# Performance work log

Measured on AMD Instinct MI355X. Metric: run time of the kernel, lower is better.

Reference implementation:

```python
import jax, jax.numpy as jnp
import numpy as np

NHEAD = 8
LN_EPS = 1e-5


def _l2norm(x, eps=1e-6):
    # matches torch.nn.functional.normalize(p=2, eps=eps)
    n = jnp.linalg.norm(x, axis=-1, keepdims=True)
    return x / jnp.maximum(n, eps)


def setup_inputs() -> dict:
    key = jax.random.key(0)
    ks = jax.random.split(key, 10)
    Q, B, D = 100, 16, 256
    T, Dc = 8192, 768
    s = lambda d: 1.0 / np.sqrt(d)
    return {
        "tgt": jax.random.normal(ks[0], (Q, B, D), jnp.float32),
        "text_classification": jax.random.normal(ks[1], (B, T, Dc), jnp.float32),
        "query_pos": jax.random.normal(ks[2], (Q, B, D), jnp.float32),
        "out_of_vocab_logits": jax.random.normal(ks[3], (B, Q, T), jnp.float32),
        "Wq": jax.random.normal(ks[4], (D, D), jnp.float32) * s(D),
        "bq": jnp.zeros((D,), jnp.float32),
        "Wk": jax.random.normal(ks[5], (D, Dc), jnp.float32) * s(Dc),
        "bk": jnp.zeros((D,), jnp.float32),
        "Wv": jax.random.normal(ks[6], (D, Dc), jnp.float32) * s(Dc),
        "bv": jnp.zeros((D,), jnp.float32),
        "Wo": jax.random.normal(ks[7], (D, D), jnp.float32) * s(D),
        "bo": jnp.zeros((D,), jnp.float32),
        "ln_g": jnp.ones((D,), jnp.float32),
        "ln_b": jnp.zeros((D,), jnp.float32),
        "log_scale": jnp.asarray(np.log(1.0 / 0.07), jnp.float32),
    }


def reference(tgt, text_classification, query_pos, out_of_vocab_logits,
              Wq, bq, Wk, bk, Wv, bv, Wo, bo, ln_g, ln_b, log_scale):
    Qn, B, D = tgt.shape
    T = text_classification.shape[1]
    H = NHEAD
    hd = D // H

    # forward_post: q = tgt + query_pos ; k = v = text_classification
    q_in = tgt + query_pos                                   # [Q, B, D]
    q = jnp.einsum('qbd,ed->qbe', q_in, Wq) + bq             # [Q, B, D]
    k = jnp.einsum('btc,ec->bte', text_classification, Wk) + bk  # [B, T, D]
    v = jnp.einsum('btc,ec->bte', text_classification, Wv) + bv  # [B, T, D]

    # split heads -> [B, H, L, hd]
    q = q.transpose(1, 0, 2).reshape(B, Qn, H, hd).transpose(0, 2, 1, 3)
    k = k.reshape(B, T, H, hd).transpose(0, 2, 1, 3)
    v = v.reshape(B, T, H, hd).transpose(0, 2, 1, 3)

    q = _l2norm(q)
    k = _l2norm(k)
    scale = jnp.minimum(jnp.exp(log_scale), 100.0)
    logits = jnp.einsum('bhqd,bhkd->bhqk', q, k) * scale     # [B, H, Q, T]

    # per-head ensemble with out-of-vocab logits
    alpha = jnp.linspace(0.0, 1.0, H, dtype=logits.dtype).reshape(1, H, 1, 1)
    logits = logits * (1.0 - alpha) + out_of_vocab_logits[:, None] * alpha

    attn = jax.nn.softmax(logits, axis=-1)
    out = jnp.einsum('bhqk,bhkd->bhqd', attn, v)             # [B, H, Q, hd]
    out = out.transpose(0, 2, 1, 3).reshape(B, Qn, D).transpose(1, 0, 2)  # [Q, B, D]
    out = jnp.einsum('qbd,ed->qbe', out, Wo) + bo

    # residual + LayerNorm (post-norm)
    x = tgt + out
    mu = x.mean(axis=-1, keepdims=True)
    var = x.var(axis=-1, keepdims=True)
    x = (x - mu) * jax.lax.rsqrt(var + LN_EPS) * ln_g + ln_b
    return x
```

## Files before the change

### kernel.cpp

```cpp
#include <hip/hip_runtime.h>
#include <hip/hip_bf16.h>

#define QN 100
#define QP 112
#define BB 16
#define DD 256
#define TT 8192
#define DC 768
#define HH 8
#define HD 32
#define NS 8
#define TSL (TT / NS)

typedef short bf16x4 __attribute__((ext_vector_type(4)));
typedef short bf16x8 __attribute__((ext_vector_type(8)));
typedef float f32x4 __attribute__((ext_vector_type(4)));

__device__ __forceinline__ uint pack_bf16_hi2(float f0, float f1) {
  return (__float_as_uint(f0) >> 16) | (__float_as_uint(f1) & 0xffff0000u);
}

__global__ __launch_bounds__(256) void qproj_kernel(
    const float* __restrict__ tgt, const float* __restrict__ qpos,
    const float* __restrict__ Wq, const float* __restrict__ bq,
    ushort* __restrict__ Qhi, ushort* __restrict__ Qlo) {
  int bid = blockIdx.x;
  int q = bid >> 4, b = bid & 15;
  int e = threadIdx.x;
  int h = e >> 5, d = e & 31;
  size_t widx = ((size_t)(b * HH + h) * QP + q) * HD + d;
  if (q >= QN) { Qhi[widx] = 0; Qlo[widx] = 0; return; }
  __shared__ float arow[DD];
  size_t off = ((size_t)q * BB + b) * DD + e;
  arow[e] = tgt[off] + qpos[off];
  __syncthreads();
  const float4* w4 = (const float4*)(Wq + (size_t)e * DD);
  const float4* a4 = (const float4*)arow;
  float acc = bq[e];
#pragma unroll 8
  for (int i = 0; i < DD / 4; ++i) {
    float4 wv = w4[i], av = a4[i];
    acc += wv.x * av.x + wv.y * av.y + wv.z * av.z + wv.w * av.w;
  }
  float ss = acc * acc;
#pragma unroll
  for (int o = 16; o; o >>= 1) ss += __shfl_xor(ss, o, 64);
  float qn = acc * (1.0f / fmaxf(sqrtf(ss), 1e-6f));
  uint u = __float_as_uint(qn);
  float hif = __uint_as_float(u & 0xffff0000u);
  Qhi[widx] = (ushort)(u >> 16);
  Qlo[widx] = (ushort)(__float_as_uint(qn - hif) >> 16);
}

__global__ __launch_bounds__(256) void kv_gemm_kernel(
    const float* __restrict__ text,
    const float* __restrict__ Wk, const float* __restrict__ bk,
    const float* __restrict__ Wv, const float* __restrict__ bv,
    float* __restrict__ Kout, float* __restrict__ Vout) {
  __shared__ short Ahi[4][129][8];
  __shared__ short Alo[4][129][8];
  __shared__ short Bhi[4][129][8];
  __shared__ short Blo[4][129][8];

  int bid = blockIdx.x;
  int w = (bid & 7) * 512 + (bid >> 3);
  int mt = w >> 2, nt = w & 3;
  int m0 = mt * 128, n0 = nt * 128;
  int tid = threadIdx.x;

  const float* Wbase = (n0 < 256) ? Wk : Wv;
  const float* bias_vec = (n0 < 256) ? bk : bv;
  float* dst = (n0 < 256) ? Kout : Vout;
  int ncol0 = n0 & 255;

  int r = tid & 127;
  bool isA = tid < 128;
  const float* src = isA ? (text + (size_t)(m0 + r) * DC)
                         : (Wbase + (size_t)(ncol0 + r) * DC);
  short (*dhi)[129][8] = isA ? Ahi : Bhi;
  short (*dlo)[129][8] = isA ? Alo : Blo;

  int lane = tid & 63, wid = tid >> 6;
  int wm = wid >> 1, wn = wid & 1;
  int kg = lane >> 4, fr = lane & 15;

  f32x4 acc[4][4];
#pragma unroll
  for (int i = 0; i < 4; ++i)
#pragma unroll
    for (int j = 0; j < 4; ++j) acc[i][j] = (f32x4){0.f, 0.f, 0.f, 0.f};

  float4 ra[8];
#pragma unroll
  for (int c = 0; c < 8; ++c) ra[c] = *(const float4*)(src + c * 4);

  for (int ks = 0; ks < DC / 32; ++ks) {
    const float* raf = (const float*)ra;
#pragma unroll
    for (int g = 0; g < 4; ++g) {
      uint hiw[4], low[4];
#pragma unroll
      for (int p = 0; p < 4; ++p) {
        float f0 = raf[8 * g + 2 * p], f1 = raf[8 * g + 2 * p + 1];
        uint b0 = __float_as_uint(f0), b1 = __float_as_uint(f1);
        float h0 = __uint_as_float(b0 & 0xffff0000u);
        float h1 = __uint_as_float(b1 & 0xffff0000u);
        hiw[p] = (b0 >> 16) | (b1 & 0xffff0000u);
        low[p] = (__float_as_uint(f0 - h0) >> 16) |
                 (__float_as_uint(f1 - h1) & 0xffff0000u);
      }
      *(uint4*)&dhi[g][r][0] = make_uint4(hiw[0], hiw[1], hiw[2], hiw[3]);
      *(uint4*)&dlo[g][r][0] = make_uint4(low[0], low[1], low[2], low[3]);
    }
    __syncthreads();

    if (ks < DC / 32 - 1) {
      const float* s2 = src + (ks + 1) * 32;
#pragma unroll
      for (int c = 0; c < 8; ++c) ra[c] = *(const float4*)(s2 + c * 4);
    }

    bf16x8 bh[4], bl[4];
#pragma unroll
    for (int ni = 0; ni < 4; ++ni) {
      int row = wn * 64 + ni * 16 + fr;
      bh[ni] = *(const bf16x8*)&Bhi[kg][row][0];
      bl[ni] = *(const bf16x8*)&Blo[kg][row][0];
    }
#pragma unroll
    for (int mi = 0; mi < 4; ++mi) {
      int row = wm * 64 + mi * 16 + fr;
      bf16x8 ah = *(const bf16x8*)&Ahi[kg][row][0];
      bf16x8 al = *(const bf16x8*)&Alo[kg][row][0];
#pragma unroll
      for (int ni = 0; ni < 4; ++ni) {
        acc[mi][ni] = __builtin_amdgcn_mfma_f32_16x16x32_bf16(
            ah, bh[ni], acc[mi][ni], 0, 0, 0);
        acc[mi][ni] = __builtin_amdgcn_mfma_f32_16x16x32_bf16(
            ah, bl[ni], acc[mi][ni], 0, 0, 0);
        acc[mi][ni] = __builtin_amdgcn_mfma_f32_16x16x32_bf16(
            al, bh[ni], acc[mi][ni], 0, 0, 0);
      }
    }
    __syncthreads();
  }

#pragma unroll
  for (int ni = 0; ni < 4; ++ni) {
    int col = n0 + wn * 64 + ni * 16 + fr;
    int e = col & 255;
    int h = e >> 5, d = e & 31;
    float bias = bias_vec[e];
#pragma unroll
    for (int mi = 0; mi < 4; ++mi) {
      f32x4 c = acc[mi][ni];
      int mbase = m0 + wm * 64 + mi * 16 + kg * 4;
#pragma unroll
      for (int j = 0; j < 4; ++j) {
        int m = mbase + j;
        int b = m >> 13, t = m & 8191;
        dst[(((size_t)(b * HH + h)) * TT + t) * HD + d] = c[j] + bias;
      }
    }
  }
}

__global__ __launch_bounds__(256) void prep_kernel(float* __restrict__ Kbuf,
                                                   float* __restrict__ Vbuf) {
  __shared__ float vl[32][257];
  int c = blockIdx.x;
  int tid = threadIdx.x;
  float* Kc = Kbuf + (size_t)c * 8192;
  float* Vc = Vbuf + (size_t)c * 8192;

  float kr[32];
#pragma unroll
  for (int i = 0; i < 8; ++i)
    *(float4*)&kr[i * 4] = *(const float4*)(Kc + (size_t)tid * 32 + i * 4);
#pragma unroll
  for (int i = 0; i < 8; ++i) {
    float4 v = *(const float4*)(Vc + (size_t)tid * 32 + i * 4);
    vl[i * 4 + 0][tid] = v.x;
    vl[i * 4 + 1][tid] = v.y;
    vl[i * 4 + 2][tid] = v.z;
    vl[i * 4 + 3][tid] = v.w;
  }
  __syncthreads();

  float ss = 0.f;
#pragma unroll
  for (int i = 0; i < 32; ++i) ss += kr[i] * kr[i];
  float rk = 1.0f / fmaxf(sqrtf(ss), 1e-6f);
  ushort* Kh = (ushort*)Kc;
  uint hiw[16], low[16];
#pragma unroll
  for (int p = 0; p < 16; ++p) {
    float f0 = kr[2 * p] * rk, f1 = kr[2 * p + 1] * rk;
    uint b0 = __float_as_uint(f0), b1 = __float_as_uint(f1);
    float h0 = __uint_as_float(b0 & 0xffff0000u);
    float h1 = __uint_as_float(b1 & 0xffff0000u);
    hiw[p] = (b0 >> 16) | (b1 & 0xffff0000u);
    low[p] = (__float_as_uint(f0 - h0) >> 16) |
             (__float_as_uint(f1 - h1) & 0xffff0000u);
  }
#pragma unroll
  for (int i = 0; i < 4; ++i) {
    *(uint4*)(Kh + (size_t)tid * 32 + i * 8) =
        make_uint4(hiw[4 * i], hiw[4 * i + 1], hiw[4 * i + 2], hiw[4 * i + 3]);
    *(uint4*)(Kh + 8192 + (size_t)tid * 32 + i * 8) =
        make_uint4(low[4 * i], low[4 * i + 1], low[4 * i + 2], low[4 * i + 3]);
  }

  int d = tid & 31, c8 = tid >> 5;
  float vv[32];
#pragma unroll
  for (int t = 0; t < 32; ++t) vv[t] = vl[d][c8 * 32 + t];
  ushort* Vh = (ushort*)Vc;
#pragma unroll
  for (int p = 0; p < 16; ++p) {
    float f0 = vv[2 * p], f1 = vv[2 * p + 1];
    uint b0 = __float_as_uint(f0), b1 = __float_as_uint(f1);
    float h0 = __uint_as_float(b0 & 0xffff0000u);
    float h1 = __uint_as_float(b1 & 0xffff0000u);
    hiw[p] = (b0 >> 16) | (b1 & 0xffff0000u);
    low[p] = (__float_as_uint(f0 - h0) >> 16) |
             (__float_as_uint(f1 - h1) & 0xffff0000u);
  }
#pragma unroll
  for (int i = 0; i < 4; ++i) {
    *(uint4*)(Vh + (size_t)d * 256 + c8 * 32 + i * 8) =
        make_uint4(hiw[4 * i], hiw[4 * i + 1], hiw[4 * i + 2], hiw[4 * i + 3]);
    *(uint4*)(Vh + 8192 + (size_t)d * 256 + c8 * 32 + i * 8) =
        make_uint4(low[4 * i], low[4 * i + 1], low[4 * i + 2], low[4 * i + 3]);
  }
}

__global__ __launch_bounds__(256, 2) void attn_kernel(
    const ushort* __restrict__ Qhi, const ushort* __restrict__ Qlo,
    const ushort* __restrict__ Kpl, const ushort* __restrict__ Vpl,
    const float* __restrict__ oov, const float* __restrict__ log_scale,
    float* __restrict__ pacc, float* __restrict__ pl) {
  __shared__ short Pbuf[4][2][QP][36];
  int bid = blockIdx.x;
  int sl = bid & 7, bh = bid >> 3;
  int b = bh >> 3, h = bh & 7;
  int tid = threadIdx.x, lane = tid & 63, w = tid >> 6;
  int fr = lane & 15, kg = lane >> 4;

  float scale = fminf(__expf(log_scale[0]), 100.0f);
  float alpha = (float)h * (1.0f / 7.0f);
  float cs = scale * (1.0f - alpha);

  bf16x8 qhf[7], qlf[7];
#pragma unroll
  for (int qt = 0; qt < 7; ++qt) {
    size_t qa = ((size_t)bh * QP + qt * 16 + fr) * HD + kg * 8;
    qhf[qt] = *(const bf16x8*)(Qhi + qa);
    qlf[qt] = *(const bf16x8*)(Qlo + qa);
  }

  f32x4 oacc[7][2];
#pragma unroll
  for (int qt = 0; qt < 7; ++qt)
#pragma unroll
    for (int dt = 0; dt < 2; ++dt) oacc[qt][dt] = (f32x4){0.f, 0.f, 0.f, 0.f};
  float lsum[7][4];
#pragma unroll
  for (int qt = 0; qt < 7; ++qt)
#pragma unroll
    for (int j = 0; j < 4; ++j) lsum[qt][j] = 0.f;

  short* Ph = &Pbuf[w][0][0][0];
  short* Pl = &Pbuf[w][1][0][0];
  const float* oovb = oov + (size_t)b * QN * TT;

  for (int s = 0; s < 8; ++s) {
    int t0 = sl * TSL + s * 128 + w * 32;
    int c = bh * 32 + (t0 >> 8);
    int ttb = t0 & 255;
    const ushort* Kc = Kpl + (size_t)c * 16384;
    const ushort* Vc = Vpl + (size_t)c * 16384;

    bf16x8 kh[2], kl[2];
#pragma unroll
    for (int tt = 0; tt < 2; ++tt) {
      int off = (ttb + tt * 16 + fr) * HD + kg * 8;
      kh[tt] = *(const bf16x8*)(Kc + off);
      kl[tt] = *(const bf16x8*)(Kc + 8192 + off);
    }

#pragma unroll
    for (int qt = 0; qt < 7; ++qt) {
#pragma unroll
      for (int tt = 0; tt < 2; ++tt) {
        f32x4 sacc = (f32x4){0.f, 0.f, 0.f, 0.f};
        sacc = __builtin_amdgcn_mfma_f32_16x16x32_bf16(qhf[qt], kh[tt], sacc, 0, 0, 0);
        sacc = __builtin_amdgcn_mfma_f32_16x16x32_bf16(qlf[qt], kh[tt], sacc, 0, 0, 0);
        sacc = __builtin_amdgcn_mfma_f32_16x16x32_bf16(qhf[qt], kl[tt], sacc, 0, 0, 0);
        int tcol = t0 + tt * 16 + fr;
#pragma unroll
        for (int j = 0; j < 4; ++j) {
          int q = qt * 16 + kg * 4 + j;
          int qc = q < QN ? q : QN - 1;
          float ov = oovb[(size_t)qc * TT + tcol];
          float S = __expf(sacc[j] * cs + ov * alpha);
          lsum[qt][j] += S;
          uint u = __float_as_uint(S);
          float hif = __uint_as_float(u & 0xffff0000u);
          Ph[q * 36 + tt * 16 + fr] = (short)(u >> 16);
          Pl[q * 36 + tt * 16 + fr] = (short)(__float_as_uint(S - hif) >> 16);
        }
      }
    }

    bf16x8 vh[2], vlo[2];
#pragma unroll
    for (int dt = 0; dt < 2; ++dt) {
      int off = (dt * 16 + fr) * 256 + ttb + kg * 8;
      vh[dt] = *(const bf16x8*)(Vc + off);
      vlo[dt] = *(const bf16x8*)(Vc + 8192 + off);
    }

#pragma unroll
    for (int qt = 0; qt < 7; ++qt) {
      int qrow = qt * 16 + fr;
      bf16x4 ph0 = *(const bf16x4*)&Ph[qrow * 36 + kg * 8];
      bf16x4 ph1 = *(const bf16x4*)&Ph[qrow * 36 + kg * 8 + 4];
      bf16x4 pl0 = *(const bf16x4*)&Pl[qrow * 36 + kg * 8];
      bf16x4 pl1 = *(const bf16x4*)&Pl[qrow * 36 + kg * 8 + 4];
      bf16x8 pా = __builtin_shufflevector(ph0, ph1, 0, 1, 2, 3, 4, 5, 6, 7);
      bf16x8 plv = __builtin_shufflevector(pl0, pl1, 0, 1, 2, 3, 4, 5, 6, 7);
#pragma unroll
      for (int dt = 0; dt < 2; ++dt) {
        oacc[qt][dt] = __builtin_amdgcn_mfma_f32_16x16x32_bf16(pా, vh[dt], oacc[qt][dt], 0, 0, 0);
        oacc[qt][dt] = __builtin_amdgcn_mfma_f32_16x16x32_bf16(plv, vh[dt], oacc[qt][dt], 0, 0, 0);
        oacc[qt][dt] = __builtin_amdgcn_mfma_f32_16x16x32_bf16(pా, vlo[dt], oacc[qt][dt], 0, 0, 0);
      }
    }
  }

#pragma unroll
  for (int qt = 0; qt < 7; ++qt)
#pragma unroll
    for (int j = 0; j < 4; ++j) {
      float v = lsum[qt][j];
      v += __shfl_xor(v, 1, 64);
      v += __shfl_xor(v, 2, 64);
      v += __shfl_xor(v, 4, 64);
      v += __shfl_xor(v, 8, 64);
      lsum[qt][j] = v;
    }

  float* red = (float*)&Pbuf[w][0][0][0];
#pragma unroll
  for (int qt = 0; qt < 7; ++qt)
#pragma unroll
    for (int dt = 0; dt < 2; ++dt)
#pragma unroll
      for (int j = 0; j < 4; ++j)
        red[(qt * 16 + kg * 4 + j) * HD + dt * 16 + fr] = oacc[qt][dt][j];
  if (fr == 0) {
#pragma unroll
    for (int qt = 0; qt < 7; ++qt)
#pragma unroll
      for (int j = 0; j < 4; ++j)
        red[QP * HD + qt * 16 + kg * 4 + j] = lsum[qt][j];
  }
  __syncthreads();

  const int WSTRIDE = 2 * QP * 36 / 2;
  float* r0 = (float*)&Pbuf[0][0][0][0];
  size_t pbase = ((size_t)bh * NS + sl) * QN;
  for (int idx = tid; idx < QN * HD; idx += 256) {
    int q = idx >> 5, d = idx & 31;
    float ssum = 0.f;
#pragma unroll
    for (int wv = 0; wv < 4; ++wv) ssum += r0[wv * WSTRIDE + (q * HD + d)];
    pacc[(pbase + q) * HD + d] = ssum;
  }
  if (tid < QN) {
    float lt = 0.f;
#pragma unroll
    for (int wv = 0; wv < 4; ++wv) lt += r0[wv * WSTRIDE + QP * HD + tid];
    pl[pbase + tid] = lt;
  }
}

__global__ __launch_bounds__(256) void out_kernel(
    const float* __restrict__ part_acc, const float* __restrict__ part_l,
    const float* __restrict__ Wo, const float* __restrict__ bo,
    const float* __restrict__ tgt, const float* __restrict__ ln_g,
    const float* __restrict__ ln_b, float* __restrict__ out) {
  int bid = blockIdx.x;
  int q = bid >> 4, b = bid & 15;
  int e = threadIdx.x;
  int h = e >> 5, d = e & 31;
  __shared__ float row[DD];
  __shared__ float r1[4], r2[4];

  size_t base = ((size_t)(b * HH + h)) * NS * QN + q;
  float a = 0.0f, lt = 0.0f;
#pragma unroll
  for (int s = 0; s < NS; ++s) {
    a += part_acc[(base + (size_t)s * QN) * HD + d];
    lt += part_l[base + (size_t)s * QN];
  }
  row[e] = a / lt;
  __syncthreads();

  const float4* w4 = (const float4*)(Wo + (size_t)e * DD);
  const float4* r4 = (const float4*)row;
  float o = bo[e];
#pragma unroll 8
  for (int i = 0; i < DD / 4; ++i) {
    float4 wv = w4[i], rv = r4[i];
    o += wv.x * rv.x + wv.y * rv.y + wv.z * rv.z + wv.w * rv.w;
  }
  float x = tgt[((size_t)q * BB + b) * DD + e] + o;

  float s1 = x, s2 = x * x;
#pragma unroll
  for (int off = 32; off; off >>= 1) {
    s1 += __shfl_xor(s1, off, 64);
    s2 += __shfl_xor(s2, off, 64);
  }
  int wid = e >> 6, lane = e & 63;
  if (lane == 0) { r1[wid] = s1; r2[wid] = s2; }
  __syncthreads();
  float T1 = r1[0] + r1[1] + r1[2] + r1[3];
  float T2 = r2[0] + r2[1] + r2[2] + r2[3];
  float mu = T1 * (1.0f / DD);
  float var = T2 * (1.0f / DD) - mu * mu;
  out[((size_t)q * BB + b) * DD + e] =
      (x - mu) * rsqrtf(var + 1e-5f) * ln_g[e] + ln_b[e];
}

extern "C" void kernel_launch(void* const* d_in, const int* in_sizes, int n_in,
                              void* d_out, int out_size, void* d_ws, size_t ws_size,
                              hipStream_t stream) {
  (void)in_sizes; (void)n_in; (void)out_size; (void)ws_size;
  const float* tgt  = (const float*)d_in[0];
  const float* text = (const float*)d_in[1];
  const float* qpos = (const float*)d_in[2];
  const float* oov  = (const float*)d_in[3];
  const float* Wq = (const float*)d_in[4];
  const float* bq = (const float*)d_in[5];
  const float* Wk = (const float*)d_in[6];
  const float* bk = (const float*)d_in[7];
  const float* Wv = (const float*)d_in[8];
  const float* bv = (const float*)d_in[9];
  const float* Wo = (const float*)d_in[10];
  const float* bo = (const float*)d_in[11];
  const float* ln_g = (const float*)d_in[12];
  const float* ln_b = (const float*)d_in[13];
  const float* log_scale = (const float*)d_in[14];
  float* out = (float*)d_out;

  char* wsb = (char*)d_ws;
  ushort* Qhi = (ushort*)wsb;
  ushort* Qlo = Qhi + (size_t)BB * HH * QP * HD;
  float* Kbuf = (float*)(wsb + 2u * 917504u);
  float* Vbuf = Kbuf + (size_t)BB * HH * TT * HD;
  float* pacc = Vbuf + (size_t)BB * HH * TT * HD;
  float* pl   = pacc + (size_t)BB * HH * NS * QN * HD;

  hipLaunchKernelGGL(qproj_kernel, dim3(QP * BB), dim3(DD), 0, stream,
                     tgt, qpos, Wq, bq, Qhi, Qlo);
  hipLaunchKernelGGL(kv_gemm_kernel, dim3(4096), dim3(256), 0, stream,
                     text, Wk, bk, Wv, bv, Kbuf, Vbuf);
  hipLaunchKernelGGL(prep_kernel, dim3(4096), dim3(256), 0, stream,
                     Kbuf, Vbuf);
  hipLaunchKernelGGL(attn_kernel, dim3(BB * HH * NS), dim3(256), 0, stream,
                     (const ushort*)Kbuf ? Qhi : Qhi, Qlo,
                     (const ushort*)Kbuf, (const ushort*)Vbuf,
                     oov, log_scale, pacc, pl);
  hipLaunchKernelGGL(out_kernel, dim3(QN * BB), dim3(DD), 0, stream,
                     pacc, pl, Wo, bo, tgt, ln_g, ln_b, out);
}
```

Baseline: 1.552 ms.

## Transpose oov to fp16, drop P low-part MFMAs, split attention finer

Adds a kernel that transposes out_of_vocab_logits into a [B,T,128] fp16 layout so the attention kernel can load it with vector reads instead of strided fp32 gathers. The attention kernel now keeps P in bf16 only, dropping the low-part MFMA and its shared-memory traffic. It also moves to 128-thread blocks with 16 T-slices and writes per-wave partials, removing the in-block reduction. The KV GEMM loop is manually double-buffered in registers. Precision drops for oov (fp16) and for P (bf16 only), and out_kernel now reduces 32 partials instead of 8.

Measured after the change: 1.385 ms. 1.12x faster.

```diff
diff --git a/kernel.cpp b/kernel.cpp
--- a/kernel.cpp
+++ b/kernel.cpp
@@ -9,16 +9,13 @@
 #define DC 768
 #define HH 8
 #define HD 32
-#define NS 8
-#define TSL (TT / NS)
+#define SL16 16
+#define NPART 32
 
 typedef short bf16x4 __attribute__((ext_vector_type(4)));
 typedef short bf16x8 __attribute__((ext_vector_type(8)));
 typedef float f32x4 __attribute__((ext_vector_type(4)));
-
-__device__ __forceinline__ uint pack_bf16_hi2(float f0, float f1) {
-  return (__float_as_uint(f0) >> 16) | (__float_as_uint(f1) & 0xffff0000u);
-}
+typedef _Float16 half4 __attribute__((ext_vector_type(4)));
 
 __global__ __launch_bounds__(256) void qproj_kernel(
     const float* __restrict__ tgt, const float* __restrict__ qpos,
@@ -52,6 +49,48 @@
   Qlo[widx] = (ushort)(__float_as_uint(qn - hif) >> 16);
 }
 
+#define KV_CONVERT(RAF)                                                       \
+  {                                                                           \
+    const float* raf = (const float*)(RAF);                                   \
+    _Pragma("unroll") for (int g = 0; g < 4; ++g) {                           \
+      uint hiw[4], low[4];                                                    \
+      _Pragma("unroll") for (int p2 = 0; p2 < 4; ++p2) {                      \
+        float f0 = raf[8 * g + 2 * p2], f1 = raf[8 * g + 2 * p2 + 1];         \
+        uint b0 = __float_as_uint(f0), b1 = __float_as_uint(f1);              \
+        float h0 = __uint_as_float(b0 & 0xffff0000u);                         \
+        float h1 = __uint_as_float(b1 & 0xffff0000u);                         \
+        hiw[p2] = (b0 >> 16) | (b1 & 0xffff0000u);                            \
+        low[p2] = (__float_as_uint(f0 - h0) >> 16) |                          \
+                  (__float_as_uint(f1 - h1) & 0xffff0000u);                   \
+      }                                                                       \
+      *(uint4*)&dhi[g][r][0] = make_uint4(hiw[0], hiw[1], hiw[2], hiw[3]);    \
+      *(uint4*)&dlo[g][r][0] = make_uint4(low[0], low[1], low[2], low[3]);    \
+    }                                                                         \
+  }
+
+#define KV_MFMA()                                                             \
+  {                                                                           \
+    bf16x8 bhf[4], blf[4];                                                    \
+    _Pragma("unroll") for (int ni = 0; ni < 4; ++ni) {                        \
+      int row = wn * 64 + ni * 16 + fr;                                       \
+      bhf[ni] = *(const bf16x8*)&Bhi[kg][row][0];                             \
+      blf[ni] = *(const bf16x8*)&Blo[kg][row][0];                             \
+    }                                                                         \
+    _Pragma("unroll") for (int mi = 0; mi < 4; ++mi) {                        \
+      int row = wm * 64 + mi * 16 + fr;                                       \
+      bf16x8 ah = *(const bf16x8*)&Ahi[kg][row][0];                           \
+      bf16x8 al = *(const bf16x8*)&Alo[kg][row][0];                           \
+      _Pragma("unroll") for (int ni = 0; ni < 4; ++ni) {                      \
+        acc[mi][ni] = __builtin_amdgcn_mfma_f32_16x16x32_bf16(                \
+            ah, bhf[ni], acc[mi][ni], 0, 0, 0);                               \
+        acc[mi][ni] = __builtin_amdgcn_mfma_f32_16x16x32_bf16(                \
+            ah, blf[ni], acc[mi][ni], 0, 0, 0);                               \
+        acc[mi][ni] = __builtin_amdgcn_mfma_f32_16x16x32_bf16(                \
+            al, bhf[ni], acc[mi][ni], 0, 0, 0);                               \
+      }                                                                       \
+    }                                                                         \
+  }
+
 __global__ __launch_bounds__(256) void kv_gemm_kernel(
     const float* __restrict__ text,
     const float* __restrict__ Wk, const float* __restrict__ bk,
@@ -90,58 +129,28 @@
 #pragma unroll
     for (int j = 0; j < 4; ++j) acc[i][j] = (f32x4){0.f, 0.f, 0.f, 0.f};
 
-  float4 ra[8];
-#pragma unroll
-  for (int c = 0; c < 8; ++c) ra[c] = *(const float4*)(src + c * 4);
-
-  for (int ks = 0; ks < DC / 32; ++ks) {
-    const float* raf = (const float*)ra;
-#pragma unroll
-    for (int g = 0; g < 4; ++g) {
-      uint hiw[4], low[4];
-#pragma unroll
-      for (int p = 0; p < 4; ++p) {
-        float f0 = raf[8 * g + 2 * p], f1 = raf[8 * g + 2 * p + 1];
-        uint b0 = __float_as_uint(f0), b1 = __float_as_uint(f1);
-        float h0 = __uint_as_float(b0 & 0xffff0000u);
-        float h1 = __uint_as_float(b1 & 0xffff0000u);
-        hiw[p] = (b0 >> 16) | (b1 & 0xffff0000u);
-        low[p] = (__float_as_uint(f0 - h0) >> 16) |
-                 (__float_as_uint(f1 - h1) & 0xffff0000u);
-      }
-      *(uint4*)&dhi[g][r][0] = make_uint4(hiw[0], hiw[1], hiw[2], hiw[3]);
-      *(uint4*)&dlo[g][r][0] = make_uint4(low[0], low[1], low[2], low[3]);
-    }
+  float4 raA[8], raB[8];
+#pragma unroll
+  for (int c = 0; c < 8; ++c) raA[c] = *(const float4*)(src + c * 4);
+
+  for (int ks = 0; ks < 24; ks += 2) {
+    {
+      const float* s2 = src + (ks + 1) * 32;
+#pragma unroll
+      for (int c = 0; c < 8; ++c) raB[c] = *(const float4*)(s2 + c * 4);
+    }
+    KV_CONVERT(raA);
     __syncthreads();
-
-    if (ks < DC / 32 - 1) {
-      const float* s2 = src + (ks + 1) * 32;
-#pragma unroll
-      for (int c = 0; c < 8; ++c) ra[c] = *(const float4*)(s2 + c * 4);
-    }
-
-    bf16x8 bh[4], bl[4];
-#pragma unroll
-    for (int ni = 0; ni < 4; ++ni) {
-      int row = wn * 64 + ni * 16 + fr;
-      bh[ni] = *(const bf16x8*)&Bhi[kg][row][0];
-      bl[ni] = *(const bf16x8*)&Blo[kg][row][0];
-    }
-#pragma unroll
-    for (int mi = 0; mi < 4; ++mi) {
-      int row = wm * 64 + mi * 16 + fr;
-      bf16x8 ah = *(const bf16x8*)&Ahi[kg][row][0];
-      bf16x8 al = *(const bf16x8*)&Alo[kg][row][0];
-#pragma unroll
-      for (int ni = 0; ni < 4; ++ni) {
-        acc[mi][ni] = __builtin_amdgcn_mfma_f32_16x16x32_bf16(
-            ah, bh[ni], acc[mi][ni], 0, 0, 0);
-        acc[mi][ni] = __builtin_amdgcn_mfma_f32_16x16x32_bf16(
-            ah, bl[ni], acc[mi][ni], 0, 0, 0);
-        acc[mi][ni] = __builtin_amdgcn_mfma_f32_16x16x32_bf16(
-            al, bh[ni], acc[mi][ni], 0, 0, 0);
-      }
-    }
+    KV_MFMA();
+    __syncthreads();
+    if (ks + 2 < 24) {
+      const float* s3 = src + (ks + 2) * 32;
+#pragma unroll
+      for (int c = 0; c < 8; ++c) raA[c] = *(const float4*)(s3 + c * 4);
+    }
+    KV_CONVERT(raB);
+    __syncthreads();
+    KV_MFMA();
     __syncthreads();
   }
 
@@ -235,14 +244,43 @@
   }
 }
 
-__global__ __launch_bounds__(256, 2) void attn_kernel(
+__global__ __launch_bounds__(256) void oovt_kernel(
+    const float* __restrict__ oov, ushort* __restrict__ oovT) {
+  __shared__ ushort tile[64][116];
+  int bidx = blockIdx.x;
+  int b = bidx >> 7, tc = (bidx & 127) * 64;
+  int tid = threadIdx.x;
+#pragma unroll
+  for (int rr = 0; rr < 25; ++rr) {
+    int idx = rr * 256 + tid;
+    int q = idx >> 6, tt = idx & 63;
+    float v = oov[((size_t)b * QN + q) * TT + tc + tt];
+    tile[tt][q] = __builtin_bit_cast(ushort, (_Float16)v);
+  }
+#pragma unroll
+  for (int rr = 0; rr < 3; ++rr) {
+    int idx = rr * 256 + tid;
+    tile[idx & 63][100 + (idx >> 6)] = 0;
+  }
+  __syncthreads();
+#pragma unroll
+  for (int rr = 0; rr < 7; ++rr) {
+    int idx = rr * 256 + tid;
+    int tt = idx / 28, jj = idx - tt * 28;
+    int q0 = jj * 4;
+    *(uint2*)(oovT + (((size_t)b * TT + tc + tt) << 7) + q0) =
+        *(const uint2*)&tile[tt][q0];
+  }
+}
+
+__global__ __launch_bounds__(128, 3) void attn_kernel(
     const ushort* __restrict__ Qhi, const ushort* __restrict__ Qlo,
     const ushort* __restrict__ Kpl, const ushort* __restrict__ Vpl,
-    const float* __restrict__ oov, const float* __restrict__ log_scale,
+    const ushort* __restrict__ oovT, const float* __restrict__ log_scale,
     float* __restrict__ pacc, float* __restrict__ pl) {
-  __shared__ short Pbuf[4][2][QP][36];
+  __shared__ short Pbuf[2][QP][36];
   int bid = blockIdx.x;
-  int sl = bid & 7, bh = bid >> 3;
+  int sl = bid & 15, bh = bid >> 4;
   int b = bh >> 3, h = bh & 7;
   int tid = threadIdx.x, lane = tid & 63, w = tid >> 6;
   int fr = lane & 15, kg = lane >> 4;
@@ -251,14 +289,6 @@
   float alpha = (float)h * (1.0f / 7.0f);
   float cs = scale * (1.0f - alpha);
 
-  bf16x8 qhf[7], qlf[7];
-#pragma unroll
-  for (int qt = 0; qt < 7; ++qt) {
-    size_t qa = ((size_t)bh * QP + qt * 16 + fr) * HD + kg * 8;
-    qhf[qt] = *(const bf16x8*)(Qhi + qa);
-    qlf[qt] = *(const bf16x8*)(Qlo + qa);
-  }
-
   f32x4 oacc[7][2];
 #pragma unroll
   for (int qt = 0; qt < 7; ++qt)
@@ -270,12 +300,11 @@
 #pragma unroll
     for (int j = 0; j < 4; ++j) lsum[qt][j] = 0.f;
 
-  short* Ph = &Pbuf[w][0][0][0];
-  short* Pl = &Pbuf[w][1][0][0];
-  const float* oovb = oov + (size_t)b * QN * TT;
+  short* Ph = &Pbuf[w][0][0];
+  const size_t qbase = (size_t)bh * QP * HD;
 
   for (int s = 0; s < 8; ++s) {
-    int t0 = sl * TSL + s * 128 + w * 32;
+    int t0 = sl * 512 + s * 64 + w * 32;
     int c = bh * 32 + (t0 >> 8);
     int ttb = t0 & 255;
     const ushort* Kc = Kpl + (size_t)c * 16384;
@@ -288,27 +317,26 @@
       kh[tt] = *(const bf16x8*)(Kc + off);
       kl[tt] = *(const bf16x8*)(Kc + 8192 + off);
     }
+    const ushort* ovb = oovT + (((size_t)b * TT + t0) << 7);
 
 #pragma unroll
     for (int qt = 0; qt < 7; ++qt) {
+      size_t qa = qbase + (size_t)(qt * 16 + fr) * HD + kg * 8;
+      bf16x8 qh = *(const bf16x8*)(Qhi + qa);
+      bf16x8 ql = *(const bf16x8*)(Qlo + qa);
 #pragma unroll
       for (int tt = 0; tt < 2; ++tt) {
         f32x4 sacc = (f32x4){0.f, 0.f, 0.f, 0.f};
-        sacc = __builtin_amdgcn_mfma_f32_16x16x32_bf16(qhf[qt], kh[tt], sacc, 0, 0, 0);
-        sacc = __builtin_amdgcn_mfma_f32_16x16x32_bf16(qlf[qt], kh[tt], sacc, 0, 0, 0);
-        sacc = __builtin_amdgcn_mfma_f32_16x16x32_bf16(qhf[qt], kl[tt], sacc, 0, 0, 0);
-        int tcol = t0 + tt * 16 + fr;
+        sacc = __builtin_amdgcn_mfma_f32_16x16x32_bf16(qh, kh[tt], sacc, 0, 0, 0);
+        sacc = __builtin_amdgcn_mfma_f32_16x16x32_bf16(ql, kh[tt], sacc, 0, 0, 0);
+        sacc = __builtin_amdgcn_mfma_f32_16x16x32_bf16(qh, kl[tt], sacc, 0, 0, 0);
+        half4 hv = *(const half4*)(ovb + (size_t)(tt * 16 + fr) * 128 + qt * 16 + kg * 4);
 #pragma unroll
         for (int j = 0; j < 4; ++j) {
-          int q = qt * 16 + kg * 4 + j;
-          int qc = q < QN ? q : QN - 1;
-          float ov = oovb[(size_t)qc * TT + tcol];
-          float S = __expf(sacc[j] * cs + ov * alpha);
-          lsum[qt][j] += S;
-          uint u = __float_as_uint(S);
-          float hif = __uint_as_float(u & 0xffff0000u);
-          Ph[q * 36 + tt * 16 + fr] = (short)(u >> 16);
-          Pl[q * 36 + tt * 16 + fr] = (short)(__float_as_uint(S - hif) >> 16);
+          float S = __expf(sacc[j] * cs + (float)hv[j] * alpha);
+          uint u = __float_as_uint(S) & 0xffff0000u;
+          lsum[qt][j] += __uint_as_float(u);
+          Ph[(qt * 16 + kg * 4 + j) * 36 + tt * 16 + fr] = (short)(u >> 16);
         }
       }
     }
@@ -320,21 +348,16 @@
       vh[dt] = *(const bf16x8*)(Vc + off);
       vlo[dt] = *(const bf16x8*)(Vc + 8192 + off);
     }
-
 #pragma unroll
     for (int qt = 0; qt < 7; ++qt) {
       int qrow = qt * 16 + fr;
-      bf16x4 ph0 = *(const bf16x4*)&Ph[qrow * 36 + kg * 8];
-      bf16x4 ph1 = *(const bf16x4*)&Ph[qrow * 36 + kg * 8 + 4];
-      bf16x4 pl0 = *(const bf16x4*)&Pl[qrow * 36 + kg * 8];
-      bf16x4 pl1 = *(const bf16x4*)&Pl[qrow * 36 + kg * 8 + 4];
-      bf16x8 pా = __builtin_shufflevector(ph0, ph1, 0, 1, 2, 3, 4, 5, 6, 7);
-      bf16x8 plv = __builtin_shufflevector(pl0, pl1, 0, 1, 2, 3, 4, 5, 6, 7);
+      bf16x4 p0 = *(const bf16x4*)&Ph[qrow * 36 + kg * 8];
+      bf16x4 p1 = *(const bf16x4*)&Ph[qrow * 36 + kg * 8 + 4];
+      bf16x8 pv8 = __builtin_shufflevector(p0, p1, 0, 1, 2, 3, 4, 5, 6, 7);
 #pragma unroll
       for (int dt = 0; dt < 2; ++dt) {
-        oacc[qt][dt] = __builtin_amdgcn_mfma_f32_16x16x32_bf16(pా, vh[dt], oacc[qt][dt], 0, 0, 0);
-        oacc[qt][dt] = __builtin_amdgcn_mfma_f32_16x16x32_bf16(plv, vh[dt], oacc[qt][dt], 0, 0, 0);
-        oacc[qt][dt] = __builtin_amdgcn_mfma_f32_16x16x32_bf16(pా, vlo[dt], oacc[qt][dt], 0, 0, 0);
+        oacc[qt][dt] = __builtin_amdgcn_mfma_f32_16x16x32_bf16(pv8, vh[dt], oacc[qt][dt], 0, 0, 0);
+        oacc[qt][dt] = __builtin_amdgcn_mfma_f32_16x16x32_bf16(pv8, vlo[dt], oacc[qt][dt], 0, 0, 0);
       }
     }
   }
@@ -350,39 +373,25 @@
       v += __shfl_xor(v, 8, 64);
       lsum[qt][j] = v;
     }
-
-  float* red = (float*)&Pbuf[w][0][0][0];
+  int ps = bh * NPART + sl * 2 + w;
+  size_t pb = (size_t)ps * QN;
 #pragma unroll
   for (int qt = 0; qt < 7; ++qt)
 #pragma unroll
     for (int dt = 0; dt < 2; ++dt)
 #pragma unroll
-      for (int j = 0; j < 4; ++j)
-        red[(qt * 16 + kg * 4 + j) * HD + dt * 16 + fr] = oacc[qt][dt][j];
+      for (int j = 0; j < 4; ++j) {
+        int q = qt * 16 + kg * 4 + j;
+        if (q < QN) pacc[(pb + q) * HD + dt * 16 + fr] = oacc[qt][dt][j];
+      }
   if (fr == 0) {
 #pragma unroll
     for (int qt = 0; qt < 7; ++qt)
 #pragma unroll
-      for (int j = 0; j < 4; ++j)
-        red[QP * HD + qt * 16 + kg * 4 + j] = lsum[qt][j];
-  }
-  __syncthreads();
-
-  const int WSTRIDE = 2 * QP * 36 / 2;
-  float* r0 = (float*)&Pbuf[0][0][0][0];
-  size_t pbase = ((size_t)bh * NS + sl) * QN;
-  for (int idx = tid; idx < QN * HD; idx += 256) {
-    int q = idx >> 5, d = idx & 31;
-    float ssum = 0.f;
-#pragma unroll
-    for (int wv = 0; wv < 4; ++wv) ssum += r0[wv * WSTRIDE + (q * HD + d)];
-    pacc[(pbase + q) * HD + d] = ssum;
-  }
-  if (tid < QN) {
-    float lt = 0.f;
-#pragma unroll
-    for (int wv = 0; wv < 4; ++wv) lt += r0[wv * WSTRIDE + QP * HD + tid];
-    pl[pbase + tid] = lt;
+      for (int j = 0; j < 4; ++j) {
+        int q = qt * 16 + kg * 4 + j;
+        if (q < QN) pl[pb + q] = lsum[qt][j];
+      }
   }
 }
 
@@ -398,10 +407,10 @@
   __shared__ float row[DD];
   __shared__ float r1[4], r2[4];
 
-  size_t base = ((size_t)(b * HH + h)) * NS * QN + q;
+  size_t base = ((size_t)(b * HH + h)) * NPART * QN + q;
   float a = 0.0f, lt = 0.0f;
-#pragma unroll
-  for (int s = 0; s < NS; ++s) {
+#pragma unroll 8
+  for (int s = 0; s < NPART; ++s) {
     a += part_acc[(base + (size_t)s * QN) * HD + d];
     lt += part_l[base + (size_t)s * QN];
   }
@@ -461,8 +470,9 @@
   ushort* Qlo = Qhi + (size_t)BB * HH * QP * HD;
   float* Kbuf = (float*)(wsb + 2u * 917504u);
   float* Vbuf = Kbuf + (size_t)BB * HH * TT * HD;
-  float* pacc = Vbuf + (size_t)BB * HH * TT * HD;
-  float* pl   = pacc + (size_t)BB * HH * NS * QN * HD;
+  ushort* oovT = (ushort*)(Vbuf + (size_t)BB * HH * TT * HD);
+  float* pacc = (float*)((char*)oovT + (size_t)BB * TT * 128 * 2);
+  float* pl   = pacc + (size_t)BB * HH * NPART * QN * HD;
 
   hipLaunchKernelGGL(qproj_kernel, dim3(QP * BB), dim3(DD), 0, stream,
                      tgt, qpos, Wq, bq, Qhi, Qlo);
@@ -470,10 +480,11 @@
                      text, Wk, bk, Wv, bv, Kbuf, Vbuf);
   hipLaunchKernelGGL(prep_kernel, dim3(4096), dim3(256), 0, stream,
                      Kbuf, Vbuf);
-  hipLaunchKernelGGL(attn_kernel, dim3(BB * HH * NS), dim3(256), 0, stream,
-                     (const ushort*)Kbuf ? Qhi : Qhi, Qlo,
-                     (const ushort*)Kbuf, (const ushort*)Vbuf,
-                     oov, log_scale, pacc, pl);
+  hipLaunchKernelGGL(oovt_kernel, dim3(BB * 128), dim3(256), 0, stream,
+                     oov, oovT);
+  hipLaunchKernelGGL(attn_kernel, dim3(BB * HH * SL16), dim3(128), 0, stream,
+                     Qhi, Qlo, (const ushort*)Kbuf, (const ushort*)Vbuf,
+                     oovT, log_scale, pacc, pl);
   hipLaunchKernelGGL(out_kernel, dim3(QN * BB), dim3(DD), 0, stream,
                      pacc, pl, Wo, bo, tgt, ln_g, ln_b, out);
 }
```
